# Kernel tuning notes

Measured on AMD Instinct MI355X. Metric: run time of the kernel, lower is better.

Reference implementation:

```python
import jax, jax.numpy as jnp
import numpy as np

DIM = 1024
HEADS = 16
HEAD_DIM = DIM // HEADS
EPS = 1e-5


def layer_norm(x, w, b):
    # normalize over last dim (head_dim)
    mu = jnp.mean(x, axis=-1, keepdims=True)
    var = jnp.mean(jnp.square(x - mu), axis=-1, keepdims=True)
    return (x - mu) * jax.lax.rsqrt(var + EPS) * w + b


def setup_inputs() -> dict:
    key = jax.random.key(0)
    ks = jax.random.split(key, 8)
    B, N = 2, 2048
    x = jax.random.normal(ks[0], (B, N, DIM), dtype=jnp.float32)
    mask = jax.random.randint(ks[1], (B, 1, N, N), 0, 2) == 1  # True = masked out
    qkv_w = jax.random.normal(ks[2], (3 * DIM, DIM), dtype=jnp.float32) * (DIM ** -0.5)
    q_norm_w = jnp.ones((HEAD_DIM,), dtype=jnp.float32)
    q_norm_b = jnp.zeros((HEAD_DIM,), dtype=jnp.float32)
    k_norm_w = jnp.ones((HEAD_DIM,), dtype=jnp.float32)
    k_norm_b = jnp.zeros((HEAD_DIM,), dtype=jnp.float32)
    proj_w = jax.random.normal(ks[3], (DIM, DIM), dtype=jnp.float32) * (DIM ** -0.5)
    proj_b = jnp.zeros((DIM,), dtype=jnp.float32)
    return {"x": x, "mask": mask, "qkv_w": qkv_w,
            "q_norm_w": q_norm_w, "q_norm_b": q_norm_b,
            "k_norm_w": k_norm_w, "k_norm_b": k_norm_b,
            "proj_w": proj_w, "proj_b": proj_b}


def reference(x, mask, qkv_w, q_norm_w, q_norm_b, k_norm_w, k_norm_b, proj_w, proj_b):
    B, N, C = x.shape
    H, D = HEADS, HEAD_DIM
    scale = D ** -0.5
    # qkv projection (no bias), split into q,k,v of shape (B,H,N,D)
    qkv = (x @ qkv_w.T).reshape(B, N, 3, H, D).transpose(2, 0, 3, 1, 4)
    q, k, v = qkv[0], qkv[1], qkv[2]
    q = layer_norm(q, q_norm_w, q_norm_b)
    k = layer_norm(k, k_norm_w, k_norm_b)
    q = q * scale
    attn = jnp.einsum("bhnd,bhmd->bhnm", q, k)  # (B,H,N,N)
    attn = jnp.where(mask, -jnp.inf, attn)
    attn = jax.nn.softmax(attn, axis=-1)
    out = jnp.einsum("bhnm,bhmd->bhnd", attn, v)
    out = out.transpose(0, 2, 1, 3).reshape(B, N, C)
    return out @ proj_w.T + proj_b
```

## Files before the change

kernel.cpp:

```cpp
#include <hip/hip_runtime.h>
#include <hip/hip_bf16.h>
#include <math.h>

#define B_    2
#define N_    2048
#define DIM_  1024
#define H_    16
#define HD_   64
#define EPS_  1e-5f
#define SCALE_ 0.125f
#define LOG2E_ 1.4426950408889634f
#define MFIX_  14.0f

typedef __attribute__((ext_vector_type(8))) __bf16 bf16x8;
typedef __attribute__((ext_vector_type(8))) unsigned short ushort8;
typedef __attribute__((ext_vector_type(4))) float f32x4;
typedef __attribute__((ext_vector_type(4))) unsigned int uint4v;

__device__ __forceinline__ unsigned short f2bf(float x) {
    unsigned u = __builtin_bit_cast(unsigned, x);
    u += 0x7fff + ((u >> 16) & 1);
    return (unsigned short)(u >> 16);
}
__device__ __forceinline__ unsigned pk2bf(float a, float b) {
    unsigned ua = __builtin_bit_cast(unsigned, a) + 0x8000u;
    unsigned ub = __builtin_bit_cast(unsigned, b) + 0x8000u;
    return __builtin_amdgcn_perm(ub, ua, 0x07060302);
}
__device__ __forceinline__ unsigned cvtpk(float a, float b) {
    unsigned r;
    asm("v_cvt_pk_bf16_f32 %0, %1, %2" : "=v"(r) : "v"(a), "v"(b));
    return r;
}

__device__ __forceinline__ void gl_lds16(const void* g, void* l) {
    __builtin_amdgcn_global_load_lds(
        (const __attribute__((address_space(1))) void*)g,
        (__attribute__((address_space(3))) void*)l, 16, 0, 0);
}

__global__ __launch_bounds__(256) void cast_all_bf16(
    const float* __restrict__ x, const float* __restrict__ qkvw,
    const float* __restrict__ pw, unsigned short* __restrict__ out) {
    int i = (blockIdx.x * 256 + threadIdx.x) * 8;
    const float* src;
    if (i < 4194304) src = x + i;
    else if (i < 7340032) src = qkvw + (i - 4194304);
    else src = pw + (i - 7340032);
    float4 v0 = *(const float4*)src;
    float4 v1 = *(const float4*)(src + 4);
    ushort8 r;
    r[0] = f2bf(v0.x); r[1] = f2bf(v0.y); r[2] = f2bf(v0.z); r[3] = f2bf(v0.w);
    r[4] = f2bf(v1.x); r[5] = f2bf(v1.y); r[6] = f2bf(v1.z); r[7] = f2bf(v1.w);
    *(ushort8*)(out + i) = r;
}

__global__ __launch_bounds__(256) void pack_mask(
    const int* __restrict__ mask, unsigned long long* __restrict__ bm) {
    int w = blockIdx.x * 4 + (threadIdx.x >> 6);
    int lane = threadIdx.x & 63;
    int mv = mask[(size_t)w * 64 + lane];
    unsigned long long bits = __ballot(mv != 0);
    if (lane == 0) bm[w] = bits;
}

__global__ __launch_bounds__(256) void gemm_qkv_ln(
    const unsigned short* __restrict__ A, const unsigned short* __restrict__ Bw,
    const float* __restrict__ qnw, const float* __restrict__ qnb,
    const float* __restrict__ knw, const float* __restrict__ knb,
    unsigned short* __restrict__ qbuf, unsigned short* __restrict__ kbuf,
    unsigned short* __restrict__ vbuf) {
    const int K = DIM_;
    __shared__ unsigned short As[128 * 32];
    __shared__ unsigned short Bs[128 * 32];
    const int tid = threadIdx.x;
    const int wave = tid >> 6, lane = tid & 63;
    const int quad = lane >> 4, lcol = lane & 15;
    const int wr = wave >> 1, wc = wave & 1;
    const int row0 = blockIdx.y * 128, col0 = blockIdx.x * 128;

    f32x4 acc[4][4];
#pragma unroll
    for (int i = 0; i < 4; ++i)
#pragma unroll
        for (int j = 0; j < 4; ++j) acc[i][j] = (f32x4){0.f, 0.f, 0.f, 0.f};

    for (int k0 = 0; k0 < K; k0 += 32) {
        __syncthreads();
#pragma unroll
        for (int c = 0; c < 2; ++c) {
            int base = wave * 2048 + c * 1024;
            int myofs = base + lane * 16;
            int r = myofs >> 6;
            int kb = myofs & 63;
            gl_lds16((const char*)A + ((size_t)(row0 + r) * K + k0) * 2 + kb,
                     (char*)As + base);
            gl_lds16((const char*)Bw + ((size_t)(col0 + r) * K + k0) * 2 + kb,
                     (char*)Bs + base);
        }
        __syncthreads();

        bf16x8 af[4], bfr[4];
#pragma unroll
        for (int i = 0; i < 4; ++i) {
            af[i] = *(const bf16x8*)&As[(wr * 64 + i * 16 + lcol) * 32 + quad * 8];
            bfr[i] = *(const bf16x8*)&Bs[(wc * 64 + i * 16 + lcol) * 32 + quad * 8];
        }
#pragma unroll
        for (int i = 0; i < 4; ++i)
#pragma unroll
            for (int j = 0; j < 4; ++j)
                acc[i][j] = __builtin_amdgcn_mfma_f32_16x16x32_bf16(
                    af[i], bfr[j], acc[i][j], 0, 0, 0);
    }

    const int colbase = col0 + wc * 64;
    const int t = colbase >> 10;
    const int h = (colbase & 1023) >> 6;

    if (t < 2) {
        const float* wv = (t == 0) ? qnw : knw;
        const float* bv = (t == 0) ? qnb : knb;
        float wreg[4], breg[4];
#pragma unroll
        for (int j = 0; j < 4; ++j) {
            wreg[j] = wv[j * 16 + lcol];
            breg[j] = bv[j * 16 + lcol];
        }
        const float sc = (t == 0) ? (SCALE_ * LOG2E_) : 1.f;
        unsigned short* obase = (t == 0) ? qbuf : kbuf;
#pragma unroll
        for (int i = 0; i < 4; ++i) {
#pragma unroll
            for (int reg = 0; reg < 4; ++reg) {
                int row = row0 + wr * 64 + i * 16 + quad * 4 + reg;
                int bb = row >> 11, n = row & (N_ - 1);
                float v[4];
#pragma unroll
                for (int j = 0; j < 4; ++j) v[j] = acc[i][j][reg];
                float s = v[0] + v[1] + v[2] + v[3];
                s += __shfl_xor(s, 1);
                s += __shfl_xor(s, 2);
                s += __shfl_xor(s, 4);
                s += __shfl_xor(s, 8);
                float mu = s * (1.f / 64.f);
                float d[4], s2 = 0.f;
#pragma unroll
                for (int j = 0; j < 4; ++j) {
                    d[j] = v[j] - mu;
                    s2 += d[j] * d[j];
                }
                s2 += __shfl_xor(s2, 1);
                s2 += __shfl_xor(s2, 2);
                s2 += __shfl_xor(s2, 4);
                s2 += __shfl_xor(s2, 8);
                float r = rsqrtf(s2 * (1.f / 64.f) + EPS_);
                float o0 = (d[0] * r * wreg[0] + breg[0]) * sc;
                float o1 = (d[1] * r * wreg[1] + breg[1]) * sc;
                float o2 = (d[2] * r * wreg[2] + breg[2]) * sc;
                float o3 = (d[3] * r * wreg[3] + breg[3]) * sc;
                uint2 pk;
                pk.x = pk2bf(o0, o1);
                pk.y = pk2bf(o2, o3);
                *(uint2*)(obase + ((size_t)(bb * H_ + h) * N_ + n) * 64 +
                          lcol * 4) = pk;
            }
        }
    } else {
#pragma unroll
        for (int i = 0; i < 4; ++i) {
#pragma unroll
            for (int reg = 0; reg < 4; ++reg) {
                int row = row0 + wr * 64 + i * 16 + quad * 4 + reg;
                uint2 pk;
                pk.x = pk2bf(acc[i][0][reg], acc[i][1][reg]);
                pk.y = pk2bf(acc[i][2][reg], acc[i][3][reg]);
                *(uint2*)(vbuf + (size_t)row * DIM_ + h * 64 + lcol * 4) = pk;
            }
        }
    }
}

__global__ __launch_bounds__(256) void gemm_proj(
    const unsigned short* __restrict__ A, const unsigned short* __restrict__ Bw,
    const float* __restrict__ bias, float* __restrict__ Cout) {
    const int K = DIM_;
    __shared__ unsigned short As[128 * 32];
    __shared__ unsigned short Bs[64 * 32];
    const int tid = threadIdx.x;
    const int wave = tid >> 6, lane = tid & 63;
    const int quad = lane >> 4, lcol = lane & 15;
    const int row0 = blockIdx.y * 128, col0 = blockIdx.x * 64;

    f32x4 acc[2][4];
#pragma unroll
    for (int i = 0; i < 2; ++i)
#pragma unroll
        for (int j = 0; j < 4; ++j) acc[i][j] = (f32x4){0.f, 0.f, 0.f, 0.f};

    for (int k0 = 0; k0 < K; k0 += 32) {
        __syncthreads();
#pragma unroll
        for (int pi = 0; pi < 3; ++pi) {
            int p = wave * 3 + pi;
            if (p < 8) {
                int base = p * 1024;
                int myofs = base + lane * 16;
                int r = myofs >> 6, kb = myofs & 63;
                gl_lds16((const char*)A + ((size_t)(row0 + r) * K + k0) * 2 + kb,
                         (char*)As + base);
            } else {
                int base = (p - 8) * 1024;
                int myofs = base + lane * 16;
                int r = myofs >> 6, kb = myofs & 63;
                gl_lds16((const char*)Bw + ((size_t)(col0 + r) * K + k0) * 2 + kb,
                         (char*)Bs + base);
            }
        }
        __syncthreads();

        bf16x8 af[2], bfr[4];
#pragma unroll
        for (int i = 0; i < 2; ++i)
            af[i] = *(const bf16x8*)&As[(wave * 32 + i * 16 + lcol) * 32 + quad * 8];
#pragma unroll
        for (int j = 0; j < 4; ++j)
            bfr[j] = *(const bf16x8*)&Bs[(j * 16 + lcol) * 32 + quad * 8];
#pragma unroll
        for (int i = 0; i < 2; ++i)
#pragma unroll
            for (int j = 0; j < 4; ++j)
                acc[i][j] = __builtin_amdgcn_mfma_f32_16x16x32_bf16(
                    af[i], bfr[j], acc[i][j], 0, 0, 0);
    }

#pragma unroll
    for (int i = 0; i < 2; ++i) {
#pragma unroll
        for (int j = 0; j < 4; ++j) {
            int col = col0 + j * 16 + lcol;
            float bv = bias[col];
#pragma unroll
            for (int reg = 0; reg < 4; ++reg) {
                int row = row0 + wave * 32 + i * 16 + quad * 4 + reg;
                Cout[(size_t)row * DIM_ + col] = acc[i][j][reg] + bv;
            }
        }
    }
}

__global__ __launch_bounds__(256) void transpose_v(
    const unsigned short* __restrict__ vbuf, unsigned short* __restrict__ vt) {
    __shared__ unsigned short Ts[64 * 65];
    const int tid = threadIdx.x;
    const int bh = blockIdx.y, n0 = blockIdx.x * 64;
    const int b = bh >> 4, h = bh & 15;
    {
        int r = tid >> 2, s = tid & 3;
        const unsigned short* src =
            vbuf + (size_t)(b * N_ + n0 + r) * DIM_ + h * 64 + s * 16;
#pragma unroll
        for (int i = 0; i < 16; ++i) {
            int p = s * 16 + i;
            int trued = (p >> 2) + (p & 3) * 16;
            Ts[r * 65 + trued] = src[i];
        }
    }
    __syncthreads();
    {
        int d = tid >> 2, kt = tid & 3;
        unsigned short* dstrow = vt + (size_t)(bh * 64 + d) * N_ + n0;
        int P = kt >> 1, t = kt & 1;
#pragma unroll
        for (int q = 0; q < 4; ++q) {
            __align__(8) unsigned short tmp4[4];
#pragma unroll
            for (int j = 0; j < 4; ++j)
                tmp4[j] = Ts[(kt * 16 + q * 4 + j) * 65 + d];
            *(uint2*)(dstrow + P * 32 + q * 8 + t * 4) = *(const uint2*)tmp4;
        }
    }
}

#define WAITBAR(Ncnt)                                                     \
    asm volatile("s_waitcnt vmcnt(" #Ncnt ")" ::: "memory");              \
    __builtin_amdgcn_s_barrier();                                         \
    __builtin_amdgcn_sched_barrier(0);

#define ISSUE2(B0, B1)                                                    \
    {                                                                     \
        gl_lds16(kp0, (char*)Ks[B0] + kld0);                              \
        gl_lds16(kp1, (char*)Ks[B0] + kld1);                              \
        gl_lds16(vp0, (char*)Vts[B0] + kld0);                             \
        gl_lds16(vp1, (char*)Vts[B0] + kld1);                             \
        gl_lds16(kp0 + 8192, (char*)Ks[B1] + kld0);                       \
        gl_lds16(kp1 + 8192, (char*)Ks[B1] + kld1);                       \
        gl_lds16(vp0 + 128, (char*)Vts[B1] + kld0);                       \
        gl_lds16(vp1 + 128, (char*)Vts[B1] + kld1);                       \
        mm0[B0] = bmq0[0]; mm1[B0] = bmq1[0];                             \
        mm0[B1] = bmq0[1]; mm1[B1] = bmq1[1];                             \
        kp0 += 16384; kp1 += 16384; vp0 += 256; vp1 += 256;               \
        bmq0 += 2; bmq1 += 2;                                             \
    }

#define QKT(J, SACC, MWA, MWB)                                            \
    {                                                                     \
        unsigned long long mqa = (MWA) >> (quad * 4);                     \
        unsigned long long mqb = (MWB) >> (quad * 4);                     \
        unsigned ml[2][2];                                                \
        ml[0][0] = (unsigned)mqa; ml[0][1] = (unsigned)(mqa >> 32);       \
        ml[1][0] = (unsigned)mqb; ml[1][1] = (unsigned)(mqb >> 32);       \
        _Pragma("unroll")                                                 \
        for (int qf = 0; qf < 2; ++qf)                                    \
            _Pragma("unroll")                                             \
            for (int kt = 0; kt < 4; ++kt) {                              \
                unsigned word = ml[qf][kt >> 1];                          \
                _Pragma("unroll")                                         \
                for (int reg = 0; reg < 4; ++reg) {                       \
                    unsigned msk = (unsigned)(((int)(word <<              \
                        (31 - ((kt & 1) * 16 + reg)))) >> 31);            \
                    SACC[qf][kt][reg] = __builtin_bit_cast(float,         \
                        (msk & 0xc61c4000u) | (~msk & 0xc1600000u));      \
                }                                                         \
            }                                                             \
        __builtin_amdgcn_s_setprio(1);                                    \
        _Pragma("unroll")                                                 \
        for (int kt = 0; kt < 4; ++kt)                                    \
            _Pragma("unroll")                                             \
            for (int d0 = 0; d0 < 2; ++d0) {                              \
                bf16x8 ak = *(const bf16x8*)((const char*)Ks[J] +         \
                    (d0 * 4 + quad) * 1024 + kt * 256 + lofs);            \
                SACC[0][kt] = __builtin_amdgcn_mfma_f32_16x16x32_bf16(    \
                    ak, bq[0][d0], SACC[0][kt], 0, 0, 0);                 \
                SACC[1][kt] = __builtin_amdgcn_mfma_f32_16x16x32_bf16(    \
                    ak, bq[1][d0], SACC[1][kt], 0, 0, 0);                 \
            }                                                             \
        __builtin_amdgcn_s_setprio(0);                                    \
    }

#define SM(SACC, PK)                                                      \
    _Pragma("unroll")                                                     \
    for (int qf = 0; qf < 2; ++qf)                                        \
        _Pragma("unroll")                                                 \
        for (int kt = 0; kt < 4; ++kt) {                                  \
            float p0 = exp2f(SACC[qf][kt][0]);                            \
            float p1 = exp2f(SACC[qf][kt][1]);                            \
            float p2 = exp2f(SACC[qf][kt][2]);                            \
            float p3 = exp2f(SACC[qf][kt][3]);                            \
            PK[qf][kt].x = cvtpk(p0, p1);                                 \
            PK[qf][kt].y = cvtpk(p2, p3);                                 \
        }

#define PV(J, PK)                                                         \
    {                                                                     \
        __builtin_amdgcn_s_setprio(1);                                    \
        _Pragma("unroll")                                                 \
        for (int P = 0; P < 2; ++P) {                                     \
            bf16x8 bp[2];                                                 \
            _Pragma("unroll")                                             \
            for (int qf = 0; qf < 2; ++qf) {                              \
                uint4v bu;                                                \
                bu[0] = PK[qf][2 * P].x;  bu[1] = PK[qf][2 * P].y;        \
                bu[2] = PK[qf][2 * P + 1].x; bu[3] = PK[qf][2 * P + 1].y; \
                bp[qf] = __builtin_bit_cast(bf16x8, bu);                  \
                lacc[qf] = __builtin_amdgcn_mfma_f32_16x16x32_bf16(       \
                    ones, bp[qf], lacc[qf], 0, 0, 0);                     \
            }                                                             \
            _Pragma("unroll")                                             \
            for (int dt = 0; dt < 4; ++dt) {                              \
                bf16x8 va = *(const bf16x8*)((const char*)Vts[J] +        \
                    (P * 4 + quad) * 1024 + dt * 256 + lofs);             \
                oacc[0][dt] = __builtin_amdgcn_mfma_f32_16x16x32_bf16(    \
                    va, bp[0], oacc[0][dt], 0, 0, 0);                     \
                oacc[1][dt] = __builtin_amdgcn_mfma_f32_16x16x32_bf16(    \
                    va, bp[1], oacc[1][dt], 0, 0, 0);                     \
            }                                                             \
        }                                                                 \
        __builtin_amdgcn_s_setprio(0);                                    \
    }

#define PAIR(J0, J1)                                                      \
    {                                                                     \
        f32x4 saccA[2][4], saccB[2][4];                                   \
        uint2 pkA[2][4], pkB[2][4];                                       \
        QKT(J0, saccA, mm0[J0], mm1[J0])                                  \
        SM(saccA, pkA)                                                    \
        QKT(J1, saccB, mm0[J1], mm1[J1])                                  \
        PV(J0, pkA)                                                       \
        SM(saccB, pkB)                                                    \
        PV(J1, pkB)                                                       \
    }

__global__ __launch_bounds__(256, 2) void flash_attn_mfma9(
    const unsigned short* __restrict__ q, const unsigned short* __restrict__ k,
    const unsigned short* __restrict__ vt,
    const unsigned long long* __restrict__ bm, unsigned short* __restrict__ ao) {
    __shared__ unsigned short Qs[128 * 64];
    __shared__ unsigned short Ks[4][64 * 64];
    __shared__ unsigned short Vts[4][64 * 64];

    const int tid = threadIdx.x;
    const int wave = tid >> 6, lane = tid & 63;
    const int quad = lane >> 4, lcol = lane & 15;
    const int bh = blockIdx.y, b = bh >> 4, h = bh & 15;
    const int q0 = blockIdx.x * 128;
    const int lofs = (lcol ^ (quad * 2)) << 4;

    const char* kgbase = (const char*)k + (size_t)bh * N_ * 128;
    const char* vtbase = (const char*)vt + (size_t)bh * 64 * N_ * 2;

    const int c0 = wave * 2, c1 = c0 + 1;
    const int swz0 = (c0 & 3) * 2, swz1 = (c1 & 3) * 2;
    const int kld0 = c0 * 1024, kld1 = c1 * 1024;
    const char* kp0 = kgbase + (lane ^ swz0) * 128 + c0 * 16;
    const char* kp1 = kgbase + (lane ^ swz1) * 128 + c1 * 16;
    const char* vp0 = vtbase + (size_t)(lane ^ swz0) * (N_ * 2) + c0 * 16;
    const char* vp1 = vtbase + (size_t)(lane ^ swz1) * (N_ * 2) + c1 * 16;

    const unsigned long long* bmq0 =
        bm + ((size_t)b * N_ + q0 + wave * 32 + lcol) * 32;
    const unsigned long long* bmq1 = bmq0 + 16 * 32;
    unsigned long long mm0[4], mm1[4];

    {
        const char* qg = (const char*)(q + (size_t)(bh * N_ + q0) * 64);
#pragma unroll
        for (int c = 0; c < 4; ++c) {
            int base = wave * 4096 + c * 1024;
            gl_lds16(qg + base + lane * 16, (char*)Qs + base);
        }
    }
    asm volatile("" ::: "memory");
    __builtin_amdgcn_sched_barrier(0);
#pragma unroll
    for (int t = 0; t < 4; ++t) {
        gl_lds16(kp0, (char*)Ks[t] + kld0);
        gl_lds16(kp1, (char*)Ks[t] + kld1);
        gl_lds16(vp0, (char*)Vts[t] + kld0);
        gl_lds16(vp1, (char*)Vts[t] + kld1);
        mm0[t] = bmq0[t];
        mm1[t] = bmq1[t];
        kp0 += 8192; kp1 += 8192; vp0 += 128; vp1 += 128;
        __builtin_amdgcn_sched_barrier(0);
    }
    bmq0 += 4; bmq1 += 4;
    asm volatile("s_waitcnt vmcnt(24)" ::: "memory");
    __builtin_amdgcn_sched_barrier(0);

    bf16x8 bq[2][2];
#pragma unroll
    for (int qf = 0; qf < 2; ++qf)
#pragma unroll
        for (int d0 = 0; d0 < 2; ++d0)
            bq[qf][d0] = *(const bf16x8*)&Qs[(wave * 32 + qf * 16 + lcol) * 64 +
                                             d0 * 32 + quad * 8];

    ushort8 ot;
#pragma unroll
    for (int i = 0; i < 8; ++i) ot[i] = 0x3F80;
    const bf16x8 ones = __builtin_bit_cast(bf16x8, ot);

    f32x4 oacc[2][4];
#pragma unroll
    for (int qf = 0; qf < 2; ++qf)
#pragma unroll
        for (int dt = 0; dt < 4; ++dt) oacc[qf][dt] = (f32x4){0.f, 0.f, 0.f, 0.f};
    f32x4 lacc[2];
    lacc[0] = (f32x4){0.f, 0.f, 0.f, 0.f};
    lacc[1] = (f32x4){0.f, 0.f, 0.f, 0.f};

    WAITBAR(12)
    PAIR(0, 1)
    for (int g = 0; g < 7; ++g) {
        WAITBAR(0)
        ISSUE2(0, 1)
        PAIR(2, 3)
        WAITBAR(0)
        ISSUE2(2, 3)
        PAIR(0, 1)
    }
    WAITBAR(0)
    PAIR(2, 3)

#pragma unroll
    for (int qf = 0; qf < 2; ++qf) {
        float inv = 1.f / lacc[qf][0];
        int row = q0 + wave * 32 + qf * 16 + lcol;
        unsigned short* dst =
            ao + ((size_t)(b * N_ + row)) * DIM_ + h * 64 + quad * 4;
#pragma unroll
        for (int dt = 0; dt < 4; ++dt) {
            uint2 pko;
            pko.x = pk2bf(oacc[qf][dt][0] * inv, oacc[qf][dt][1] * inv);
            pko.y = pk2bf(oacc[qf][dt][2] * inv, oacc[qf][dt][3] * inv);
            *(uint2*)(dst + dt * 16) = pko;
        }
    }
}

extern "C" void kernel_launch(void* const* d_in, const int* in_sizes, int n_in,
                              void* d_out, int out_size, void* d_ws,
                              size_t ws_size, hipStream_t stream) {
    const float* x     = (const float*)d_in[0];
    const int*   mask  = (const int*)d_in[1];
    const float* qkv_w = (const float*)d_in[2];
    const float* qnw   = (const float*)d_in[3];
    const float* qnb   = (const float*)d_in[4];
    const float* knw   = (const float*)d_in[5];
    const float* knb   = (const float*)d_in[6];
    const float* pw    = (const float*)d_in[7];
    const float* pb    = (const float*)d_in[8];
    float* out = (float*)d_out;

    char* ws = (char*)d_ws;
    unsigned short* x_bf  = (unsigned short*)(ws + 0);
    unsigned short* qw_bf = (unsigned short*)(ws + 8388608);
    unsigned short* pw_bf = (unsigned short*)(ws + 14680064);
    unsigned short* qbuf  = (unsigned short*)(ws + 16777216);
    unsigned short* kbuf  = (unsigned short*)(ws + 25165824);
    unsigned short* vbuf  = (unsigned short*)(ws + 33554432);
    unsigned short* vt    = (unsigned short*)(ws + 41943040);
    unsigned long long* bmask = (unsigned long long*)(ws + 50331648);
    unsigned short* ao_bnc = vbuf;

    cast_all_bf16<<<8388608 / 2048, 256, 0, stream>>>(x, qkv_w, pw, x_bf);

    gemm_qkv_ln<<<dim3(3072 / 128, 4096 / 128), 256, 0, stream>>>(
        x_bf, qw_bf, qnw, qnb, knw, knb, qbuf, kbuf, vbuf);

    transpose_v<<<dim3(N_ / 64, B_ * H_), 256, 0, stream>>>(vbuf, vt);

    pack_mask<<<(B_ * N_ * (N_ / 64)) / 4, 256, 0, stream>>>(mask, bmask);

    flash_attn_mfma9<<<dim3(N_ / 128, B_ * H_), 256, 0, stream>>>(
        qbuf, kbuf, vt, bmask, ao_bnc);

    gemm_proj<<<dim3(DIM_ / 64, 4096 / 128), 256, 0, stream>>>(
        ao_bnc, pw_bf, pb, out);
}
```

Measured before the change: 273.5 us.

## Fuse V transpose into QKV GEMM epilogue and shrink attention blocks

The QKV GEMM epilogue now writes V directly in transposed (head, dim, token) layout, so the separate transpose_v kernel and its extra global round trip go away. The attention kernel moves from 256-thread blocks with 128 query rows and a 4-deep K/V buffer to 128-thread blocks with 64 query rows and double buffering. It also remaps block ids to group heads, which should give more blocks, better occupancy, and more L2 reuse of K/V across neighbouring blocks. The transposed V stores are scattered 8-byte writes with large strides, which may reduce store efficiency in the GEMM. The shallower prefetch may also expose more memory latency.

```diff
diff --git a/kernel.cpp b/kernel.cpp
--- a/kernel.cpp
+++ b/kernel.cpp
@@ -69,7 +69,7 @@
     const float* __restrict__ qnw, const float* __restrict__ qnb,
     const float* __restrict__ knw, const float* __restrict__ knb,
     unsigned short* __restrict__ qbuf, unsigned short* __restrict__ kbuf,
-    unsigned short* __restrict__ vbuf) {
+    unsigned short* __restrict__ vt) {
     const int K = DIM_;
     __shared__ unsigned short As[128 * 32];
     __shared__ unsigned short Bs[128 * 32];
@@ -167,15 +167,19 @@
             }
         }
     } else {
+        const int rowb = row0 + wr * 64;
+        const int bb = rowb >> 11;
+        unsigned short* vtb =
+            vt + ((size_t)(bb * H_ + h) * 64) * (size_t)N_ + (rowb & (N_ - 1));
 #pragma unroll
         for (int i = 0; i < 4; ++i) {
-#pragma unroll
-            for (int reg = 0; reg < 4; ++reg) {
-                int row = row0 + wr * 64 + i * 16 + quad * 4 + reg;
+            const int pos = (i >> 1) * 32 + quad * 8 + (i & 1) * 4;
+#pragma unroll
+            for (int jj = 0; jj < 4; ++jj) {
                 uint2 pk;
-                pk.x = pk2bf(acc[i][0][reg], acc[i][1][reg]);
-                pk.y = pk2bf(acc[i][2][reg], acc[i][3][reg]);
-                *(uint2*)(vbuf + (size_t)row * DIM_ + h * 64 + lcol * 4) = pk;
+                pk.x = pk2bf(acc[i][jj][0], acc[i][jj][1]);
+                pk.y = pk2bf(acc[i][jj][2], acc[i][jj][3]);
+                *(uint2*)(vtb + (size_t)(lcol + 16 * jj) * N_ + pos) = pk;
             }
         }
     }
@@ -249,58 +253,26 @@
     }
 }
 
-__global__ __launch_bounds__(256) void transpose_v(
-    const unsigned short* __restrict__ vbuf, unsigned short* __restrict__ vt) {
-    __shared__ unsigned short Ts[64 * 65];
-    const int tid = threadIdx.x;
-    const int bh = blockIdx.y, n0 = blockIdx.x * 64;
-    const int b = bh >> 4, h = bh & 15;
-    {
-        int r = tid >> 2, s = tid & 3;
-        const unsigned short* src =
-            vbuf + (size_t)(b * N_ + n0 + r) * DIM_ + h * 64 + s * 16;
-#pragma unroll
-        for (int i = 0; i < 16; ++i) {
-            int p = s * 16 + i;
-            int trued = (p >> 2) + (p & 3) * 16;
-            Ts[r * 65 + trued] = src[i];
-        }
-    }
-    __syncthreads();
-    {
-        int d = tid >> 2, kt = tid & 3;
-        unsigned short* dstrow = vt + (size_t)(bh * 64 + d) * N_ + n0;
-        int P = kt >> 1, t = kt & 1;
-#pragma unroll
-        for (int q = 0; q < 4; ++q) {
-            __align__(8) unsigned short tmp4[4];
-#pragma unroll
-            for (int j = 0; j < 4; ++j)
-                tmp4[j] = Ts[(kt * 16 + q * 4 + j) * 65 + d];
-            *(uint2*)(dstrow + P * 32 + q * 8 + t * 4) = *(const uint2*)tmp4;
-        }
-    }
-}
-
-#define WAITBAR(Ncnt)                                                     \
-    asm volatile("s_waitcnt vmcnt(" #Ncnt ")" ::: "memory");              \
+#define WB0                                                               \
+    asm volatile("s_waitcnt vmcnt(0)" ::: "memory");                      \
     __builtin_amdgcn_s_barrier();                                         \
     __builtin_amdgcn_sched_barrier(0);
 
-#define ISSUE2(B0, B1)                                                    \
+#define FISSUE(BUF, M0, M1)                                               \
     {                                                                     \
-        gl_lds16(kp0, (char*)Ks[B0] + kld0);                              \
-        gl_lds16(kp1, (char*)Ks[B0] + kld1);                              \
-        gl_lds16(vp0, (char*)Vts[B0] + kld0);                             \
-        gl_lds16(vp1, (char*)Vts[B0] + kld1);                             \
-        gl_lds16(kp0 + 8192, (char*)Ks[B1] + kld0);                       \
-        gl_lds16(kp1 + 8192, (char*)Ks[B1] + kld1);                       \
-        gl_lds16(vp0 + 128, (char*)Vts[B1] + kld0);                       \
-        gl_lds16(vp1 + 128, (char*)Vts[B1] + kld1);                       \
-        mm0[B0] = bmq0[0]; mm1[B0] = bmq1[0];                             \
-        mm0[B1] = bmq0[1]; mm1[B1] = bmq1[1];                             \
-        kp0 += 16384; kp1 += 16384; vp0 += 256; vp1 += 256;               \
-        bmq0 += 2; bmq1 += 2;                                             \
+        gl_lds16(kp0, (char*)Ks[BUF] + kld0);                             \
+        gl_lds16(kp1, (char*)Ks[BUF] + kld1);                             \
+        gl_lds16(kp2, (char*)Ks[BUF] + kld2);                             \
+        gl_lds16(kp3, (char*)Ks[BUF] + kld3);                             \
+        gl_lds16(vp0, (char*)Vts[BUF] + kld0);                            \
+        gl_lds16(vp1, (char*)Vts[BUF] + kld1);                            \
+        gl_lds16(vp2, (char*)Vts[BUF] + kld2);                            \
+        gl_lds16(vp3, (char*)Vts[BUF] + kld3);                            \
+        M0 = *bmq0; M1 = *bmq1;                                           \
+        kp0 += 8192; kp1 += 8192; kp2 += 8192; kp3 += 8192;               \
+        vp0 += 128; vp1 += 128; vp2 += 128; vp3 += 128;                   \
+        ++bmq0; ++bmq1;                                                   \
+        __builtin_amdgcn_sched_barrier(0);                                \
     }
 
 #define QKT(J, SACC, MWA, MWB)                                            \
@@ -379,48 +351,50 @@
         __builtin_amdgcn_s_setprio(0);                                    \
     }
 
-#define PAIR(J0, J1)                                                      \
+#define TILE(J, M0, M1)                                                   \
     {                                                                     \
-        f32x4 saccA[2][4], saccB[2][4];                                   \
-        uint2 pkA[2][4], pkB[2][4];                                       \
-        QKT(J0, saccA, mm0[J0], mm1[J0])                                  \
-        SM(saccA, pkA)                                                    \
-        QKT(J1, saccB, mm0[J1], mm1[J1])                                  \
-        PV(J0, pkA)                                                       \
-        SM(saccB, pkB)                                                    \
-        PV(J1, pkB)                                                       \
-    }
-
-__global__ __launch_bounds__(256, 2) void flash_attn_mfma9(
+        f32x4 saccT[2][4];                                                \
+        uint2 pkT[2][4];                                                  \
+        QKT(J, saccT, M0, M1)                                             \
+        SM(saccT, pkT)                                                    \
+        PV(J, pkT)                                                        \
+    }
+
+__global__ __launch_bounds__(128, 2) void flash_attn_mfma10(
     const unsigned short* __restrict__ q, const unsigned short* __restrict__ k,
     const unsigned short* __restrict__ vt,
     const unsigned long long* __restrict__ bm, unsigned short* __restrict__ ao) {
-    __shared__ unsigned short Qs[128 * 64];
-    __shared__ unsigned short Ks[4][64 * 64];
-    __shared__ unsigned short Vts[4][64 * 64];
+    __shared__ unsigned short Qs[64 * 64];
+    __shared__ unsigned short Ks[2][64 * 64];
+    __shared__ unsigned short Vts[2][64 * 64];
 
     const int tid = threadIdx.x;
     const int wave = tid >> 6, lane = tid & 63;
     const int quad = lane >> 4, lcol = lane & 15;
-    const int bh = blockIdx.y, b = bh >> 4, h = bh & 15;
-    const int q0 = blockIdx.x * 128;
+    const int lid = blockIdx.y * 32 + blockIdx.x;
+    const int bh = (lid & 7) * 4 + ((lid >> 3) & 3);
+    const int q0 = (lid >> 5) * 64;
+    const int b = bh >> 4, h = bh & 15;
     const int lofs = (lcol ^ (quad * 2)) << 4;
 
     const char* kgbase = (const char*)k + (size_t)bh * N_ * 128;
     const char* vtbase = (const char*)vt + (size_t)bh * 64 * N_ * 2;
 
-    const int c0 = wave * 2, c1 = c0 + 1;
-    const int swz0 = (c0 & 3) * 2, swz1 = (c1 & 3) * 2;
-    const int kld0 = c0 * 1024, kld1 = c1 * 1024;
-    const char* kp0 = kgbase + (lane ^ swz0) * 128 + c0 * 16;
-    const char* kp1 = kgbase + (lane ^ swz1) * 128 + c1 * 16;
-    const char* vp0 = vtbase + (size_t)(lane ^ swz0) * (N_ * 2) + c0 * 16;
-    const char* vp1 = vtbase + (size_t)(lane ^ swz1) * (N_ * 2) + c1 * 16;
+    const int kld0 = (wave * 4 + 0) * 1024, kld1 = (wave * 4 + 1) * 1024;
+    const int kld2 = (wave * 4 + 2) * 1024, kld3 = (wave * 4 + 3) * 1024;
+    const char* kp0 = kgbase + (lane ^ 0) * 128 + (wave * 4 + 0) * 16;
+    const char* kp1 = kgbase + (lane ^ 2) * 128 + (wave * 4 + 1) * 16;
+    const char* kp2 = kgbase + (lane ^ 4) * 128 + (wave * 4 + 2) * 16;
+    const char* kp3 = kgbase + (lane ^ 6) * 128 + (wave * 4 + 3) * 16;
+    const char* vp0 = vtbase + (size_t)(lane ^ 0) * (N_ * 2) + (wave * 4 + 0) * 16;
+    const char* vp1 = vtbase + (size_t)(lane ^ 2) * (N_ * 2) + (wave * 4 + 1) * 16;
+    const char* vp2 = vtbase + (size_t)(lane ^ 4) * (N_ * 2) + (wave * 4 + 2) * 16;
+    const char* vp3 = vtbase + (size_t)(lane ^ 6) * (N_ * 2) + (wave * 4 + 3) * 16;
 
     const unsigned long long* bmq0 =
         bm + ((size_t)b * N_ + q0 + wave * 32 + lcol) * 32;
     const unsigned long long* bmq1 = bmq0 + 16 * 32;
-    unsigned long long mm0[4], mm1[4];
+    unsigned long long mA0, mA1, mB0, mB1;
 
     {
         const char* qg = (const char*)(q + (size_t)(bh * N_ + q0) * 64);
@@ -432,19 +406,8 @@
     }
     asm volatile("" ::: "memory");
     __builtin_amdgcn_sched_barrier(0);
-#pragma unroll
-    for (int t = 0; t < 4; ++t) {
-        gl_lds16(kp0, (char*)Ks[t] + kld0);
-        gl_lds16(kp1, (char*)Ks[t] + kld1);
-        gl_lds16(vp0, (char*)Vts[t] + kld0);
-        gl_lds16(vp1, (char*)Vts[t] + kld1);
-        mm0[t] = bmq0[t];
-        mm1[t] = bmq1[t];
-        kp0 += 8192; kp1 += 8192; vp0 += 128; vp1 += 128;
-        __builtin_amdgcn_sched_barrier(0);
-    }
-    bmq0 += 4; bmq1 += 4;
-    asm volatile("s_waitcnt vmcnt(24)" ::: "memory");
+    FISSUE(0, mA0, mA1)
+    asm volatile("s_waitcnt vmcnt(10)" ::: "memory");
     __builtin_amdgcn_sched_barrier(0);
 
     bf16x8 bq[2][2];
@@ -469,18 +432,12 @@
     lacc[0] = (f32x4){0.f, 0.f, 0.f, 0.f};
     lacc[1] = (f32x4){0.f, 0.f, 0.f, 0.f};
 
-    WAITBAR(12)
-    PAIR(0, 1)
-    for (int g = 0; g < 7; ++g) {
-        WAITBAR(0)
-        ISSUE2(0, 1)
-        PAIR(2, 3)
-        WAITBAR(0)
-        ISSUE2(2, 3)
-        PAIR(0, 1)
-    }
-    WAITBAR(0)
-    PAIR(2, 3)
+    for (int g = 0; g < 15; ++g) {
+        WB0 FISSUE(1, mB0, mB1) TILE(0, mA0, mA1)
+        WB0 FISSUE(0, mA0, mA1) TILE(1, mB0, mB1)
+    }
+    WB0 FISSUE(1, mB0, mB1) TILE(0, mA0, mA1)
+    WB0 TILE(1, mB0, mB1)
 
 #pragma unroll
     for (int qf = 0; qf < 2; ++qf) {
@@ -518,21 +475,18 @@
     unsigned short* pw_bf = (unsigned short*)(ws + 14680064);
     unsigned short* qbuf  = (unsigned short*)(ws + 16777216);
     unsigned short* kbuf  = (unsigned short*)(ws + 25165824);
-    unsigned short* vbuf  = (unsigned short*)(ws + 33554432);
+    unsigned short* ao_bnc= (unsigned short*)(ws + 33554432);
     unsigned short* vt    = (unsigned short*)(ws + 41943040);
     unsigned long long* bmask = (unsigned long long*)(ws + 50331648);
-    unsigned short* ao_bnc = vbuf;
 
     cast_all_bf16<<<8388608 / 2048, 256, 0, stream>>>(x, qkv_w, pw, x_bf);
 
+    pack_mask<<<(B_ * N_ * (N_ / 64)) / 4, 256, 0, stream>>>(mask, bmask);
+
     gemm_qkv_ln<<<dim3(3072 / 128, 4096 / 128), 256, 0, stream>>>(
-        x_bf, qw_bf, qnw, qnb, knw, knb, qbuf, kbuf, vbuf);
-
-    transpose_v<<<dim3(N_ / 64, B_ * H_), 256, 0, stream>>>(vbuf, vt);
-
-    pack_mask<<<(B_ * N_ * (N_ / 64)) / 4, 256, 0, stream>>>(mask, bmask);
-
-    flash_attn_mfma9<<<dim3(N_ / 128, B_ * H_), 256, 0, stream>>>(
+        x_bf, qw_bf, qnw, qnb, knw, knb, qbuf, kbuf, vt);
+
+    flash_attn_mfma10<<<dim3(32, 32), 128, 0, stream>>>(
         qbuf, kbuf, vt, bmask, ao_bnc);
 
     gemm_proj<<<dim3(DIM_ / 64, 4096 / 128), 256, 0, stream>>>(
```

Result: no change. 274.3 us (+0.3%).
